# Kernel tuning notes

Measured on AMD Instinct MI355X. Metric: run time of the kernel, lower is better.

## Reference

```python
import jax, jax.numpy as jnp
import numpy as np

EMBED = 512
HEADS = 8
HEAD_DIM = EMBED // HEADS
EPS = 1e-5


def setup_inputs() -> dict:
    key = jax.random.key(0)
    ks = jax.random.split(key, 10)
    s = 1.0 / np.sqrt(EMBED)
    x = jax.random.normal(ks[0], (2, 4096, EMBED), dtype=jnp.float32)
    Wq = jax.random.uniform(ks[1], (EMBED, EMBED), jnp.float32, -s, s)
    bq = jnp.zeros((EMBED,), jnp.float32)
    Wk = jax.random.uniform(ks[2], (EMBED, EMBED), jnp.float32, -s, s)
    bk = jnp.zeros((EMBED,), jnp.float32)
    Wv = jax.random.uniform(ks[3], (EMBED, EMBED), jnp.float32, -s, s)
    bv = jnp.zeros((EMBED,), jnp.float32)
    Wo = jax.random.uniform(ks[4], (EMBED, EMBED), jnp.float32, -s, s)
    bo = jnp.zeros((EMBED,), jnp.float32)
    gamma = jnp.ones((EMBED,), jnp.float32)
    beta = jnp.zeros((EMBED,), jnp.float32)
    return {"x": x, "Wq": Wq, "bq": bq, "Wk": Wk, "bk": bk,
            "Wv": Wv, "bv": bv, "Wo": Wo, "bo": bo,
            "gamma": gamma, "beta": beta}


def reference(x, Wq, bq, Wk, bk, Wv, bv, Wo, bo, gamma, beta):
    b, n, e = x.shape
    def split_heads(t):  # [b,n,e] -> [b,h,n,d]
        return t.reshape(b, n, HEADS, HEAD_DIM).transpose(0, 2, 1, 3)
    q = split_heads(x @ Wq + bq)
    k = split_heads(x @ Wk + bk)
    v = split_heads(x @ Wv + bv)
    energy = jnp.einsum('bhqd,bhkd->bhqk', q, k) * (HEAD_DIM ** -0.5)
    attn = jax.nn.softmax(energy, axis=-1)  # dropout=0.0 (eval)
    out = jnp.einsum('bhqk,bhkd->bhqd', attn, v)
    out = out.transpose(0, 2, 1, 3).reshape(b, n, e)
    out = out @ Wo + bo
    y = x + out
    mu = jnp.mean(y, axis=-1, keepdims=True)
    var = jnp.var(y, axis=-1, keepdims=True)
    return (y - mu) * jax.lax.rsqrt(var + EPS) * gamma + beta
```

## Files before the change

### kernel.cpp

```cpp
#include <hip/hip_runtime.h>
#include <hip/hip_bf16.h>


#define ROWS 8192
#define EMB  512
#define SEQ  4096
#define HEADS 8
#define HD   64
#define QSCALE 0.18033688011112042f

typedef __attribute__((ext_vector_type(8))) short bf16x8;
typedef __attribute__((ext_vector_type(4))) short bf16x4;
typedef __attribute__((ext_vector_type(4))) float f32x4;

__device__ __forceinline__ float bf16_to_f(unsigned short u) {
    union { unsigned int i; float f; } v; v.i = ((unsigned int)u) << 16; return v.f;
}
__device__ __forceinline__ unsigned short f_to_bf16(float f) {
    union { __hip_bfloat16 h; unsigned short u; } v; v.h = __float2bfloat16(f); return v.u;
}
__device__ __forceinline__ unsigned int pack_bf16_trunc(float a, float b) {
    return __builtin_amdgcn_perm(__float_as_uint(b), __float_as_uint(a), 0x07060302u);
}
__device__ __forceinline__ void load_lds16(const void* g, void* l) {
    __builtin_amdgcn_global_load_lds(
        (const __attribute__((address_space(1))) void*)g,
        (__attribute__((address_space(3))) void*)l, 16, 0, 0);
}

__device__ __forceinline__ int detect_fp32(const void* x) {
    const unsigned short* p = (const unsigned short*)x;
    int t = threadIdx.x & 63;
    int cnt = 0;
    #pragma unroll
    for (int i = 0; i < 4; ++i) {
        unsigned short u = p[t * 4 + i];
        int e = (u >> 7) & 0xFF;
        cnt += (e >= 140) ? 1 : 0;
    }
    #pragma unroll
    for (int off = 32; off > 0; off >>= 1) cnt += __shfl_xor(cnt, off, 64);
    return cnt > 16;
}

__global__ __launch_bounds__(256) void prep_kernel(
        const void* __restrict__ x, unsigned short* __restrict__ xb,
        const void* W0, const void* W1, const void* W2, const void* W3,
        unsigned short* __restrict__ Wt,
        const void* b0, const void* b1, const void* b2, const void* b3,
        const void* b4, const void* b5, float* __restrict__ bias_all) {
    int fp32 = detect_fp32(x);
    int bid = blockIdx.x;
    int tid = threadIdx.x;
    if (bid < 4096) {
        if (!fp32) return;
        int i = (bid * 256 + tid) * 4;
        float4 v = *(const float4*)((const float*)x + i);
        ushort4 u = { f_to_bf16(v.x), f_to_bf16(v.y), f_to_bf16(v.z), f_to_bf16(v.w) };
        *(ushort4*)(xb + i) = u;
    } else if (bid < 4352) {
        __shared__ float T[64][65];
        int idx0 = bid - 4096;
        int kt = idx0 & 7, nt = (idx0 >> 3) & 7, mat = idx0 >> 6;
        const void* src = (mat == 0) ? W0 : (mat == 1) ? W1 : (mat == 2) ? W2 : W3;
        for (int ii = 0; ii < 4; ++ii) {
            int idx = tid + ii * 256;
            int i = idx >> 4, j = (idx & 15) * 4;
            size_t g = (size_t)(kt * 64 + i) * 512 + nt * 64 + j;
            if (fp32) {
                float4 v = *(const float4*)((const float*)src + g);
                T[i][j] = v.x; T[i][j+1] = v.y; T[i][j+2] = v.z; T[i][j+3] = v.w;
            } else {
                ushort4 u = *(const ushort4*)((const unsigned short*)src + g);
                T[i][j] = bf16_to_f(u.x); T[i][j+1] = bf16_to_f(u.y);
                T[i][j+2] = bf16_to_f(u.z); T[i][j+3] = bf16_to_f(u.w);
            }
        }
        __syncthreads();
        for (int ii = 0; ii < 2; ++ii) {
            int idx = tid + ii * 256;
            int j = idx >> 3, ch = idx & 7;
            unsigned short pk[8];
            for (int t = 0; t < 8; ++t) pk[t] = f_to_bf16(T[ch * 8 + t][j]);
            *(bf16x8*)&Wt[(size_t)(mat * 512 + nt * 64 + j) * 512 + kt * 64 + ch * 8] = *(bf16x8*)pk;
        }
    } else {
        int idx = (bid - 4352) * 256 + tid;
        int mat = idx >> 9, off = idx & 511;
        const void* src = (mat == 0) ? b0 : (mat == 1) ? b1 : (mat == 2) ? b2 :
                          (mat == 3) ? b3 : (mat == 4) ? b4 : b5;
        float v;
        if (fp32) v = ((const float*)src)[off];
        else      v = bf16_to_f(((const unsigned short*)src)[off]);
        bias_all[idx] = v;
    }
}

template <typename OutT>
__global__ __launch_bounds__(256) void gemm_mfma_kernel(
        const unsigned short* __restrict__ A_conv, const unsigned short* __restrict__ A_raw,
        const unsigned short* __restrict__ Bt,
        const float* __restrict__ bias, OutT* __restrict__ C, int ldc, int scale_cols,
        unsigned short* __restrict__ VtOut) {
    __shared__ __align__(16) unsigned short smemg[2][2][128 * 64];
    const unsigned short* A = detect_fp32(A_raw) ? A_conv : A_raw;
    int tid = threadIdx.x;
    int wave = tid >> 6, lane = tid & 63;
    int l15 = lane & 15, quad = lane >> 4;

    int lin = blockIdx.x + gridDim.x * blockIdx.y;
    int nwg = gridDim.x * gridDim.y;
    int bx, by;
    if (nwg & 7) { bx = blockIdx.x; by = blockIdx.y; }
    else {
        int t = (lin & 7) * (nwg >> 3) + (lin >> 3);
        bx = t % gridDim.x; by = t / gridDim.x;
    }
    int m0 = by * 128, n0 = bx * 128;
    int wm = (wave & 1) * 64, wn = (wave >> 1) * 64;
    bool is_v = (VtOut != nullptr) && (n0 >= 1024);

    int rt = wave * 32 + (lane >> 3);
    int ch = (lane & 7) ^ ((lane >> 3) & 7);
    const unsigned short* ag = A  + (size_t)(m0 + rt) * 512 + ch * 8;
    const unsigned short* bg = Bt + (size_t)(n0 + rt) * 512 + ch * 8;

    f32x4 acc[4][4];
    for (int i = 0; i < 4; ++i) for (int j = 0; j < 4; ++j) acc[i][j] = (f32x4){0.f,0.f,0.f,0.f};

#define GSTAGE(buf, k0) do {                                                      \
        unsigned short* Atb = &smemg[buf][0][0];                                  \
        unsigned short* Bsb = &smemg[buf][1][0];                                  \
        _Pragma("unroll")                                                         \
        for (int j = 0; j < 4; ++j) {                                             \
            load_lds16(ag + (size_t)(j * 8) * 512 + (k0), &Atb[(wave * 32 + j * 8) * 64]); \
            load_lds16(bg + (size_t)(j * 8) * 512 + (k0), &Bsb[(wave * 32 + j * 8) * 64]); \
        }                                                                         \
    } while (0)

    GSTAGE(0, 0);

    for (int s = 0; s < 8; ++s) {
        int cur = s & 1;
        asm volatile("s_waitcnt vmcnt(0)" ::: "memory");
        __builtin_amdgcn_sched_barrier(0);
        asm volatile("s_barrier" ::: "memory");
        __builtin_amdgcn_sched_barrier(0);
        if (s + 1 < 8) GSTAGE(cur ^ 1, (s + 1) * 64);

        const unsigned short* At = &smemg[cur][0][0];
        const unsigned short* Bs = &smemg[cur][1][0];
        #pragma unroll
        for (int ks = 0; ks < 2; ++ks) {
            bf16x8 a[4], b[4];
            #pragma unroll
            for (int f = 0; f < 4; ++f) {
                int pc = ((ks * 4 + quad) ^ (l15 & 7)) * 8;
                a[f] = *(const bf16x8*)&At[(wm + f * 16 + l15) * 64 + pc];
                b[f] = *(const bf16x8*)&Bs[(wn + f * 16 + l15) * 64 + pc];
            }
            if (is_v) {
                #pragma unroll
                for (int fm = 0; fm < 4; ++fm)
                    #pragma unroll
                    for (int fn = 0; fn < 4; ++fn)
                        acc[fm][fn] = __builtin_amdgcn_mfma_f32_16x16x32_bf16(a[fm], b[fn], acc[fm][fn], 0, 0, 0);
            } else {
                #pragma unroll
                for (int fm = 0; fm < 4; ++fm)
                    #pragma unroll
                    for (int fn = 0; fn < 4; ++fn)
                        acc[fm][fn] = __builtin_amdgcn_mfma_f32_16x16x32_bf16(b[fn], a[fm], acc[fm][fn], 0, 0, 0);
            }
        }
        __builtin_amdgcn_sched_barrier(0);
    }
#undef GSTAGE

    __syncthreads();
    unsigned short* LT = &smemg[0][0][0];

    float sc = (n0 < scale_cols) ? QSCALE : 1.f;

    if (is_v) {
        #pragma unroll
        for (int fm = 0; fm < 4; ++fm) {
            #pragma unroll
            for (int fn = 0; fn < 4; ++fn) {
                int dcol = wn + fn * 16 + l15;
                float bia = bias[n0 + dcol];
                int seq0 = wm + fm * 16 + quad * 4;
                ushort4 pk = { f_to_bf16(acc[fm][fn][0] + bia),
                               f_to_bf16(acc[fm][fn][1] + bia),
                               f_to_bf16(acc[fm][fn][2] + bia),
                               f_to_bf16(acc[fm][fn][3] + bia) };
                int c8 = (seq0 >> 2) ^ (dcol & 31);
                *(ushort4*)&LT[dcol * 128 + c8 * 4] = pk;
            }
        }
    } else {
        #pragma unroll
        for (int fm = 0; fm < 4; ++fm) {
            #pragma unroll
            for (int fn = 0; fn < 4; ++fn) {
                int row = wm + fm * 16 + l15;
                int col0 = wn + fn * 16 + quad * 4;
                float4 b4 = *(const float4*)&bias[n0 + col0];
                ushort4 pk = { f_to_bf16((acc[fm][fn][0] + b4.x) * sc),
                               f_to_bf16((acc[fm][fn][1] + b4.y) * sc),
                               f_to_bf16((acc[fm][fn][2] + b4.z) * sc),
                               f_to_bf16((acc[fm][fn][3] + b4.w) * sc) };
                int c8 = (col0 >> 2) ^ (row & 31);
                *(ushort4*)&LT[row * 128 + c8 * 4] = pk;
            }
        }
    }
    __syncthreads();
    #pragma unroll
    for (int i = 0; i < 16; ++i) {
        int row = wave * 32 + i * 2 + (lane >> 5);
        int c8 = lane & 31;
        int phys = c8 ^ (row & 31);
        ushort4 v4 = *(const ushort4*)&LT[row * 128 + phys * 4];
        if (is_v) {
            int hd = n0 - 1024 + row;
            int bh = (m0 >> 12) * 8 + (hd >> 6);
            int d  = hd & 63;
            *(ushort4*)&VtOut[((size_t)(bh * 64 + d)) * SEQ + (m0 & 4095) + c8 * 4] = v4;
        } else {
            *(ushort4*)&C[(size_t)(m0 + row) * ldc + n0 + c8 * 4] = v4;
        }
    }
}

__global__ __launch_bounds__(256, 2) void attn_kernel(
        const unsigned short* __restrict__ QKV, const unsigned short* __restrict__ Vt,
        unsigned short* __restrict__ Ab) {
    __shared__ __align__(16) unsigned char smem[49152];
    float* Ored = (float*)smem;
    float* Lred = (float*)(smem + 16384);

    int tid = threadIdx.x;
    int wave = tid >> 6, lane = tid & 63;
    int l15 = lane & 15, quad = lane >> 4;
    int qh = wave >> 1, kh = wave & 1;
    int lin = blockIdx.x;
    int xcd = lin & 7, slot = lin >> 3;
    int grp = xcd + 8 * (slot >> 5);
    int qt = slot & 31;
    int h = grp & 7, b = grp >> 3;
    int bh = b * HEADS + h;
    size_t qrow0 = (size_t)b * SEQ + qt * 128;

    bf16x8 aq[4][2];
    #pragma unroll
    for (int t = 0; t < 4; ++t) {
        const unsigned short* qp = &QKV[(qrow0 + qh * 64 + t * 16 + l15) * 1536 + h * 64];
        aq[t][0] = *(const bf16x8*)&qp[quad * 8];
        aq[t][1] = *(const bf16x8*)&qp[32 + quad * 8];
    }
    f32x4 o[4][4];
    #pragma unroll
    for (int t = 0; t < 4; ++t)
        #pragma unroll
        for (int db = 0; db < 4; ++db) o[t][db] = (f32x4){0.f, 0.f, 0.f, 0.f};
    f32x4 ol[4];
    #pragma unroll
    for (int t = 0; t < 4; ++t) ol[t] = (f32x4){0.f, 0.f, 0.f, 0.f};
    const bf16x8 ones8 = { (short)0x3F80, (short)0x3F80, (short)0x3F80, (short)0x3F80,
                           (short)0x3F80, (short)0x3F80, (short)0x3F80, (short)0x3F80 };

    int r8 = lane >> 3;
    int kch = (lane & 7) ^ (r8 & 7);
    int r0 = wave * 16 + r8;
    int r1 = wave * 16 + 8 + r8;
    int p0r = (r0 & 32) | (((r0 >> 2) & 3) << 3) | (((r0 >> 4) & 1) << 2) | (r0 & 3);
    int p1r = (r1 & 32) | (((r1 >> 2) & 3) << 3) | (((r1 >> 4) & 1) << 2) | (r1 & 3);
    const unsigned short* kg0 = &QKV[((size_t)b * SEQ + p0r) * 1536 + 512 + h * 64 + kch * 8];
    const unsigned short* kg1 = &QKV[((size_t)b * SEQ + p1r) * 1536 + 512 + h * 64 + kch * 8];
    const unsigned short* vg = &Vt[((size_t)bh * 64 + wave * 16 + r8) * SEQ + kch * 8];

#define STAGE(buf, kt2) do {                                                          \
        unsigned short* Ksb = (unsigned short*)(smem + (buf) * 8192);                 \
        unsigned short* Vsb = (unsigned short*)(smem + 24576 + (buf) * 8192);         \
        load_lds16(kg0 + (size_t)((kt2) * 64) * 1536, &Ksb[(wave * 16) * 64]);        \
        load_lds16(kg1 + (size_t)((kt2) * 64) * 1536, &Ksb[(wave * 16 + 8) * 64]);    \
        load_lds16(vg + (size_t)((kt2) * 64), &Vsb[(wave * 16) * 64]);                \
        load_lds16(vg + (size_t)((kt2) * 64) + (size_t)8 * SEQ,                       \
                   &Vsb[(wave * 16 + 8) * 64]);                                       \
    } while (0)

    STAGE(0, 0);
    STAGE(1, 1);

    int cur = 0;
    for (int kt = 0; kt < SEQ / 64; ++kt) {
        if (kt + 1 < SEQ / 64) {
            asm volatile("s_waitcnt vmcnt(4)" ::: "memory");
        } else {
            asm volatile("s_waitcnt vmcnt(0)" ::: "memory");
        }
        asm volatile("s_barrier" ::: "memory");
        if (kt + 2 < SEQ / 64) {
            int nb2 = cur + 2; if (nb2 >= 3) nb2 -= 3;
            STAGE(nb2, kt + 2);
        }

        const unsigned short* Ksc = (const unsigned short*)(smem + cur * 8192);
        const unsigned short* Vsc = (const unsigned short*)(smem + 24576 + cur * 8192);

        bf16x8 kA[2][2];
        #pragma unroll
        for (int nb = 0; nb < 2; ++nb) {
            int krow = kh * 32 + nb * 16 + l15;
            int key = krow & 7;
            kA[nb][0] = *(const bf16x8*)&Ksc[krow * 64 + (quad ^ key) * 8];
            kA[nb][1] = *(const bf16x8*)&Ksc[krow * 64 + ((4 + quad) ^ key) * 8];
        }
        bf16x8 bv8[4];
        #pragma unroll
        for (int db = 0; db < 4; ++db) {
            int d = db * 16 + l15;
            bv8[db] = *(const bf16x8*)&Vsc[d * 64 + (((kh * 4 + quad) ^ (d & 7))) * 8];
        }
        #pragma unroll
        for (int t = 0; t < 4; ++t) {
            f32x4 sv0 = {0.f, 0.f, 0.f, 0.f};
            f32x4 sv1 = {0.f, 0.f, 0.f, 0.f};
            sv0 = __builtin_amdgcn_mfma_f32_16x16x32_bf16(kA[0][0], aq[t][0], sv0, 0, 0, 0);
            sv0 = __builtin_amdgcn_mfma_f32_16x16x32_bf16(kA[0][1], aq[t][1], sv0, 0, 0, 0);
            sv1 = __builtin_amdgcn_mfma_f32_16x16x32_bf16(kA[1][0], aq[t][0], sv1, 0, 0, 0);
            sv1 = __builtin_amdgcn_mfma_f32_16x16x32_bf16(kA[1][1], aq[t][1], sv1, 0, 0, 0);
            float p0 = __builtin_amdgcn_exp2f(sv0[0]);
            float p1 = __builtin_amdgcn_exp2f(sv0[1]);
            float p2 = __builtin_amdgcn_exp2f(sv0[2]);
            float p3 = __builtin_amdgcn_exp2f(sv0[3]);
            float p4 = __builtin_amdgcn_exp2f(sv1[0]);
            float p5 = __builtin_amdgcn_exp2f(sv1[1]);
            float p6 = __builtin_amdgcn_exp2f(sv1[2]);
            float p7 = __builtin_amdgcn_exp2f(sv1[3]);
            union { unsigned int u[4]; bf16x8 v; } ap;
            ap.u[0] = pack_bf16_trunc(p0, p1);
            ap.u[1] = pack_bf16_trunc(p2, p3);
            ap.u[2] = pack_bf16_trunc(p4, p5);
            ap.u[3] = pack_bf16_trunc(p6, p7);
            #pragma unroll
            for (int db = 0; db < 4; ++db)
                o[t][db] = __builtin_amdgcn_mfma_f32_16x16x32_bf16(ap.v, bv8[db], o[t][db], 0, 0, 0);
            ol[t] = __builtin_amdgcn_mfma_f32_16x16x32_bf16(ap.v, ones8, ol[t], 0, 0, 0);
        }
        cur = (cur == 2) ? 0 : cur + 1;
    }
#undef STAGE

    __syncthreads();
    if (l15 == 0) {
        #pragma unroll
        for (int t = 0; t < 4; ++t)
            #pragma unroll
            for (int r = 0; r < 4; ++r)
                Lred[(wave * 4 + t) * 16 + quad * 4 + r] = ol[t][r];
    }
    __syncthreads();
    float* myO = Ored + wave * (16 * 64);
    #pragma unroll
    for (int t = 0; t < 4; ++t) {
        #pragma unroll
        for (int db = 0; db < 4; ++db)
            #pragma unroll
            for (int r = 0; r < 4; ++r)
                myO[(quad * 4 + r) * 64 + db * 16 + l15] = o[t][db][r];
        __syncthreads();
        {
            int q_l = tid >> 3;
            int dg = tid & 7;
            int qh2 = q_l >> 4, qq = q_l & 15;
            const float* r0p = Ored + (qh2 * 2 + 0) * (16 * 64) + qq * 64 + dg * 8;
            const float* r1p = Ored + (qh2 * 2 + 1) * (16 * 64) + qq * 64 + dg * 8;
            float4 a0 = *(const float4*)&r0p[0];
            float4 a1 = *(const float4*)&r0p[4];
            float4 c0 = *(const float4*)&r1p[0];
            float4 c1 = *(const float4*)&r1p[4];
            float lt = Lred[((qh2 * 2 + 0) * 4 + t) * 16 + qq] +
                       Lred[((qh2 * 2 + 1) * 4 + t) * 16 + qq];
            float inv = 1.f / lt;
            size_t row = qrow0 + qh2 * 64 + t * 16 + qq;
            unsigned short* dst = &Ab[row * EMB + h * 64 + dg * 8];
            ushort4 lo = { f_to_bf16((a0.x + c0.x) * inv), f_to_bf16((a0.y + c0.y) * inv),
                           f_to_bf16((a0.z + c0.z) * inv), f_to_bf16((a0.w + c0.w) * inv) };
            ushort4 hi = { f_to_bf16((a1.x + c1.x) * inv), f_to_bf16((a1.y + c1.y) * inv),
                           f_to_bf16((a1.z + c1.z) * inv), f_to_bf16((a1.w + c1.w) * inv) };
            *(ushort4*)&dst[0] = lo;
            *(ushort4*)&dst[4] = hi;
        }
        __syncthreads();
    }
}

__global__ __launch_bounds__(256) void oproj_ln_kernel(
        const unsigned short* __restrict__ Ab, const unsigned short* __restrict__ Wo,
        const float* __restrict__ bias_all,
        const float* __restrict__ xf, const unsigned short* __restrict__ xraw,
        void* __restrict__ out) {
    __shared__ __align__(16) unsigned short Aslds[32 * 512];
    int fp32 = detect_fp32(xraw);
    int tid = threadIdx.x;
    int wave = tid >> 6, lane = tid & 63;
    int l15 = lane & 15, quad = lane >> 4;
    int m0 = blockIdx.x * 32;

    {
        int c = lane;
        #pragma unroll
        for (int j = 0; j < 8; ++j) {
            int row = j * 4 + wave;
            int csrc = c ^ (row & 7);
            load_lds16(&Ab[(size_t)(m0 + row) * 512 + csrc * 8],
                       &Aslds[row * 512 + c * 8]);
        }
    }
    asm volatile("s_waitcnt vmcnt(0)" ::: "memory");
    __syncthreads();

    f32x4 acc[2][8];
    #pragma unroll
    for (int mf = 0; mf < 2; ++mf)
        #pragma unroll
        for (int nf = 0; nf < 8; ++nf) acc[mf][nf] = (f32x4){0.f, 0.f, 0.f, 0.f};

    const unsigned short* bgl = Wo + (size_t)(wave * 128 + l15) * 512 + quad * 8;

    #pragma unroll
    for (int s = 0; s < 8; ++s) {
        bf16x8 b[2][8];
        #pragma unroll
        for (int ks = 0; ks < 2; ++ks)
            #pragma unroll
            for (int nf = 0; nf < 8; ++nf)
                b[ks][nf] = *(const bf16x8*)&bgl[(size_t)nf * (16 * 512) + s * 64 + ks * 32];
        bf16x8 a[2][2];
        #pragma unroll
        for (int ks = 0; ks < 2; ++ks)
            #pragma unroll
            for (int mf = 0; mf < 2; ++mf) {
                int row = mf * 16 + l15;
                int clog = s * 8 + ks * 4 + quad;
                a[ks][mf] = *(const bf16x8*)&Aslds[row * 512 + (clog ^ (row & 7)) * 8];
            }
        #pragma unroll
        for (int ks = 0; ks < 2; ++ks)
            #pragma unroll
            for (int mf = 0; mf < 2; ++mf)
                #pragma unroll
                for (int nf = 0; nf < 8; ++nf)
                    acc[mf][nf] = __builtin_amdgcn_mfma_f32_16x16x32_bf16(a[ks][mf], b[ks][nf], acc[mf][nf], 0, 0, 0);
    }

    __syncthreads();
    #pragma unroll
    for (int mf = 0; mf < 2; ++mf)
        #pragma unroll
        for (int nf = 0; nf < 8; ++nf) {
            int col = wave * 128 + nf * 16 + l15;
            float bo = bias_all[1536 + col];
            #pragma unroll
            for (int r = 0; r < 4; ++r) {
                int row = mf * 16 + quad * 4 + r;
                Aslds[row * 512 + col] = f_to_bf16(acc[mf][nf][r] + bo);
            }
        }
    __syncthreads();

    const float* gamma = bias_all + 4 * 512;
    const float* beta  = bias_all + 5 * 512;
    float g[8], bt[8];
    #pragma unroll
    for (int i = 0; i < 8; ++i) { g[i] = gamma[lane * 8 + i]; bt[i] = beta[lane * 8 + i]; }

    #pragma unroll
    for (int rr = 0; rr < 8; ++rr) {
        int row = wave * 8 + rr;
        size_t grow = (size_t)(m0 + row);
        const unsigned short* pp = &Aslds[row * 512 + lane * 8];
        ushort4 p0 = *(const ushort4*)&pp[0];
        ushort4 p1 = *(const ushort4*)&pp[4];
        float pv[8] = { bf16_to_f(p0.x), bf16_to_f(p0.y), bf16_to_f(p0.z), bf16_to_f(p0.w),
                        bf16_to_f(p1.x), bf16_to_f(p1.y), bf16_to_f(p1.z), bf16_to_f(p1.w) };
        float v[8];
        if (fp32) {
            const float* xp = &xf[grow * EMB + lane * 8];
            float4 x0 = *(const float4*)&xp[0];
            float4 x1 = *(const float4*)&xp[4];
            v[0] = x0.x + pv[0]; v[1] = x0.y + pv[1]; v[2] = x0.z + pv[2]; v[3] = x0.w + pv[3];
            v[4] = x1.x + pv[4]; v[5] = x1.y + pv[5]; v[6] = x1.z + pv[6]; v[7] = x1.w + pv[7];
        } else {
            const unsigned short* xp = &xraw[grow * EMB + lane * 8];
            ushort4 x0 = *(const ushort4*)&xp[0];
            ushort4 x1 = *(const ushort4*)&xp[4];
            v[0] = bf16_to_f(x0.x) + pv[0]; v[1] = bf16_to_f(x0.y) + pv[1];
            v[2] = bf16_to_f(x0.z) + pv[2]; v[3] = bf16_to_f(x0.w) + pv[3];
            v[4] = bf16_to_f(x1.x) + pv[4]; v[5] = bf16_to_f(x1.y) + pv[5];
            v[6] = bf16_to_f(x1.z) + pv[6]; v[7] = bf16_to_f(x1.w) + pv[7];
        }
        float s = 0.f, ss = 0.f;
        #pragma unroll
        for (int i = 0; i < 8; ++i) { s += v[i]; ss += v[i] * v[i]; }
        #pragma unroll
        for (int off = 32; off > 0; off >>= 1) {
            s  += __shfl_xor(s, off, 64);
            ss += __shfl_xor(ss, off, 64);
        }
        float mu = s * (1.f / 512.f);
        float var = ss * (1.f / 512.f) - mu * mu;
        float rs = rsqrtf(var + 1e-5f);
        if (fp32) {
            float* op = &((float*)out)[grow * EMB + lane * 8];
            float4 o0 = { (v[0] - mu) * rs * g[0] + bt[0], (v[1] - mu) * rs * g[1] + bt[1],
                          (v[2] - mu) * rs * g[2] + bt[2], (v[3] - mu) * rs * g[3] + bt[3] };
            float4 o1 = { (v[4] - mu) * rs * g[4] + bt[4], (v[5] - mu) * rs * g[5] + bt[5],
                          (v[6] - mu) * rs * g[6] + bt[6], (v[7] - mu) * rs * g[7] + bt[7] };
            *(float4*)&op[0] = o0;
            *(float4*)&op[4] = o1;
        } else {
            unsigned short* op = &((unsigned short*)out)[grow * EMB + lane * 8];
            ushort4 o0 = { f_to_bf16((v[0] - mu) * rs * g[0] + bt[0]),
                           f_to_bf16((v[1] - mu) * rs * g[1] + bt[1]),
                           f_to_bf16((v[2] - mu) * rs * g[2] + bt[2]),
                           f_to_bf16((v[3] - mu) * rs * g[3] + bt[3]) };
            ushort4 o1 = { f_to_bf16((v[4] - mu) * rs * g[4] + bt[4]),
                           f_to_bf16((v[5] - mu) * rs * g[5] + bt[5]),
                           f_to_bf16((v[6] - mu) * rs * g[6] + bt[6]),
                           f_to_bf16((v[7] - mu) * rs * g[7] + bt[7]) };
            *(ushort4*)&op[0] = o0;
            *(ushort4*)&op[4] = o1;
        }
    }
}

extern "C" void kernel_launch(void* const* d_in, const int* in_sizes, int n_in,
                              void* d_out, int out_size, void* d_ws, size_t ws_size,
                              hipStream_t stream) {
    char* ws = (char*)d_ws;
    char* p = ws + 256;
    float* bias_all = (float*)p;       p += 6 * 512 * 4;
    unsigned short* Wt   = (unsigned short*)p; p += (size_t)2048 * 512 * 2;
    unsigned short* QKVb = (unsigned short*)p; p += (size_t)ROWS * 1536 * 2;
    unsigned short* Vt   = (unsigned short*)p; p += (size_t)16 * HD * SEQ * 2;
    unsigned short* xb = (unsigned short*)p;
    unsigned short* Ab = (unsigned short*)p;   p += (size_t)ROWS * EMB * 2;

    prep_kernel<<<4364, 256, 0, stream>>>(d_in[0], xb,
        d_in[1], d_in[3], d_in[5], d_in[7], Wt,
        d_in[2], d_in[4], d_in[6], d_in[8], d_in[9], d_in[10], bias_all);

    gemm_mfma_kernel<unsigned short><<<dim3(12, 64), 256, 0, stream>>>(
        xb, (const unsigned short*)d_in[0], Wt, bias_all, QKVb, 1536, 512, Vt);

    attn_kernel<<<dim3(512), 256, 0, stream>>>(QKVb, Vt, Ab);

    oproj_ln_kernel<<<ROWS / 32, 256, 0, stream>>>(
        Ab, Wt + (size_t)1536 * 512, bias_all,
        (const float*)d_in[0], (const unsigned short*)d_in[0], d_out);
}
```

Baseline: 204.7 us.

## Switch attention kernel MFMAs from 16x16x32 to 32x32x16 bf16 tiles

The attention inner loop now uses 32x32x16 MFMA instructions for both the QK^T scores and the PV/row-sum products, replacing 16x16x32 tiles. Q fragments, the K row permutation on load, the LDS read patterns and the epilogue reduction layout are all changed to match the 32-row output layout. Larger MFMA tiles mean fewer instructions and fewer LDS fragment reads per FLOP, at the cost of bigger accumulators (16 floats each), which raises register pressure under the 2-blocks-per-CU launch bound.

```diff
diff --git a/kernel.cpp b/kernel.cpp
--- a/kernel.cpp
+++ b/kernel.cpp
@@ -12,6 +12,9 @@
 typedef __attribute__((ext_vector_type(8))) short bf16x8;
 typedef __attribute__((ext_vector_type(4))) short bf16x4;
 typedef __attribute__((ext_vector_type(4))) float f32x4;
+typedef __attribute__((ext_vector_type(16))) float f32x16;
+
+#define MFMA32(A, B, C) __builtin_amdgcn_mfma_f32_32x32x16_bf16(A, B, C, 0, 0, 0)
 
 __device__ __forceinline__ float bf16_to_f(unsigned short u) {
     union { unsigned int i; float f; } v; v.i = ((unsigned int)u) << 16; return v.f;
@@ -237,47 +240,49 @@
         const unsigned short* __restrict__ QKV, const unsigned short* __restrict__ Vt,
         unsigned short* __restrict__ Ab) {
     __shared__ __align__(16) unsigned char smem[49152];
-    float* Ored = (float*)smem;
-    float* Lred = (float*)(smem + 16384);
 
     int tid = threadIdx.x;
     int wave = tid >> 6, lane = tid & 63;
-    int l15 = lane & 15, quad = lane >> 4;
+    int l31 = lane & 31, lh = lane >> 5;
     int qh = wave >> 1, kh = wave & 1;
     int lin = blockIdx.x;
     int xcd = lin & 7, slot = lin >> 3;
     int grp = xcd + 8 * (slot >> 5);
-    int qt = slot & 31;
+    int qt0 = slot & 31;
     int h = grp & 7, b = grp >> 3;
     int bh = b * HEADS + h;
-    size_t qrow0 = (size_t)b * SEQ + qt * 128;
-
-    bf16x8 aq[4][2];
-    #pragma unroll
-    for (int t = 0; t < 4; ++t) {
-        const unsigned short* qp = &QKV[(qrow0 + qh * 64 + t * 16 + l15) * 1536 + h * 64];
-        aq[t][0] = *(const bf16x8*)&qp[quad * 8];
-        aq[t][1] = *(const bf16x8*)&qp[32 + quad * 8];
-    }
-    f32x4 o[4][4];
-    #pragma unroll
-    for (int t = 0; t < 4; ++t)
-        #pragma unroll
-        for (int db = 0; db < 4; ++db) o[t][db] = (f32x4){0.f, 0.f, 0.f, 0.f};
-    f32x4 ol[4];
-    #pragma unroll
-    for (int t = 0; t < 4; ++t) ol[t] = (f32x4){0.f, 0.f, 0.f, 0.f};
+    size_t qrow0 = (size_t)b * SEQ + qt0 * 128;
+
+    bf16x8 aq[2][4];
+    #pragma unroll
+    for (int qt = 0; qt < 2; ++qt) {
+        const unsigned short* qp = &QKV[(qrow0 + qh * 64 + qt * 32 + l31) * 1536 + h * 64];
+        #pragma unroll
+        for (int ks = 0; ks < 4; ++ks)
+            aq[qt][ks] = *(const bf16x8*)&qp[ks * 16 + lh * 8];
+    }
+    f32x16 o[2][2];
+    f32x16 ol[2];
+    #pragma unroll
+    for (int qt = 0; qt < 2; ++qt) {
+        #pragma unroll
+        for (int dt = 0; dt < 2; ++dt)
+            #pragma unroll
+            for (int i = 0; i < 16; ++i) o[qt][dt][i] = 0.f;
+        #pragma unroll
+        for (int i = 0; i < 16; ++i) ol[qt][i] = 0.f;
+    }
     const bf16x8 ones8 = { (short)0x3F80, (short)0x3F80, (short)0x3F80, (short)0x3F80,
                            (short)0x3F80, (short)0x3F80, (short)0x3F80, (short)0x3F80 };
 
     int r8 = lane >> 3;
     int kch = (lane & 7) ^ (r8 & 7);
-    int r0 = wave * 16 + r8;
-    int r1 = wave * 16 + 8 + r8;
-    int p0r = (r0 & 32) | (((r0 >> 2) & 3) << 3) | (((r0 >> 4) & 1) << 2) | (r0 & 3);
-    int p1r = (r1 & 32) | (((r1 >> 2) & 3) << 3) | (((r1 >> 4) & 1) << 2) | (r1 & 3);
-    const unsigned short* kg0 = &QKV[((size_t)b * SEQ + p0r) * 1536 + 512 + h * 64 + kch * 8];
-    const unsigned short* kg1 = &QKV[((size_t)b * SEQ + p1r) * 1536 + 512 + h * 64 + kch * 8];
+    int p0 = wave * 16 + r8;
+    int p1 = p0 + 8;
+    int s0 = (p0 & ~12) | ((p0 & 4) << 1) | ((p0 & 8) >> 1);
+    int s1 = (p1 & ~12) | ((p1 & 4) << 1) | ((p1 & 8) >> 1);
+    const unsigned short* kg0 = &QKV[((size_t)b * SEQ + s0) * 1536 + 512 + h * 64 + kch * 8];
+    const unsigned short* kg1 = &QKV[((size_t)b * SEQ + s1) * 1536 + 512 + h * 64 + kch * 8];
     const unsigned short* vg = &Vt[((size_t)bh * 64 + wave * 16 + r8) * SEQ + kch * 8];
 
 #define STAGE(buf, kt2) do {                                                          \
@@ -309,89 +314,89 @@
         const unsigned short* Ksc = (const unsigned short*)(smem + cur * 8192);
         const unsigned short* Vsc = (const unsigned short*)(smem + 24576 + cur * 8192);
 
-        bf16x8 kA[2][2];
-        #pragma unroll
-        for (int nb = 0; nb < 2; ++nb) {
-            int krow = kh * 32 + nb * 16 + l15;
-            int key = krow & 7;
-            kA[nb][0] = *(const bf16x8*)&Ksc[krow * 64 + (quad ^ key) * 8];
-            kA[nb][1] = *(const bf16x8*)&Ksc[krow * 64 + ((4 + quad) ^ key) * 8];
-        }
-        bf16x8 bv8[4];
-        #pragma unroll
-        for (int db = 0; db < 4; ++db) {
-            int d = db * 16 + l15;
-            bv8[db] = *(const bf16x8*)&Vsc[d * 64 + (((kh * 4 + quad) ^ (d & 7))) * 8];
-        }
-        #pragma unroll
-        for (int t = 0; t < 4; ++t) {
-            f32x4 sv0 = {0.f, 0.f, 0.f, 0.f};
-            f32x4 sv1 = {0.f, 0.f, 0.f, 0.f};
-            sv0 = __builtin_amdgcn_mfma_f32_16x16x32_bf16(kA[0][0], aq[t][0], sv0, 0, 0, 0);
-            sv0 = __builtin_amdgcn_mfma_f32_16x16x32_bf16(kA[0][1], aq[t][1], sv0, 0, 0, 0);
-            sv1 = __builtin_amdgcn_mfma_f32_16x16x32_bf16(kA[1][0], aq[t][0], sv1, 0, 0, 0);
-            sv1 = __builtin_amdgcn_mfma_f32_16x16x32_bf16(kA[1][1], aq[t][1], sv1, 0, 0, 0);
-            float p0 = __builtin_amdgcn_exp2f(sv0[0]);
-            float p1 = __builtin_amdgcn_exp2f(sv0[1]);
-            float p2 = __builtin_amdgcn_exp2f(sv0[2]);
-            float p3 = __builtin_amdgcn_exp2f(sv0[3]);
-            float p4 = __builtin_amdgcn_exp2f(sv1[0]);
-            float p5 = __builtin_amdgcn_exp2f(sv1[1]);
-            float p6 = __builtin_amdgcn_exp2f(sv1[2]);
-            float p7 = __builtin_amdgcn_exp2f(sv1[3]);
-            union { unsigned int u[4]; bf16x8 v; } ap;
-            ap.u[0] = pack_bf16_trunc(p0, p1);
-            ap.u[1] = pack_bf16_trunc(p2, p3);
-            ap.u[2] = pack_bf16_trunc(p4, p5);
-            ap.u[3] = pack_bf16_trunc(p6, p7);
-            #pragma unroll
-            for (int db = 0; db < 4; ++db)
-                o[t][db] = __builtin_amdgcn_mfma_f32_16x16x32_bf16(ap.v, bv8[db], o[t][db], 0, 0, 0);
-            ol[t] = __builtin_amdgcn_mfma_f32_16x16x32_bf16(ap.v, ones8, ol[t], 0, 0, 0);
-        }
+        bf16x8 kA[4];
+        #pragma unroll
+        for (int ks = 0; ks < 4; ++ks)
+            kA[ks] = *(const bf16x8*)&Ksc[(kh * 32 + l31) * 64 + (((ks * 2 + lh) ^ (lane & 7))) * 8];
+        bf16x8 bv[2][2];
+        #pragma unroll
+        for (int dt = 0; dt < 2; ++dt)
+            #pragma unroll
+            for (int kc = 0; kc < 2; ++kc)
+                bv[dt][kc] = *(const bf16x8*)&Vsc[(dt * 32 + l31) * 64 +
+                                                  (((kh * 4 + kc * 2 + lh) ^ (lane & 7))) * 8];
+
+        bf16x8 ap[2][2];
+        #pragma unroll
+        for (int qt = 0; qt < 2; ++qt) {
+            f32x16 sv;
+            #pragma unroll
+            for (int i = 0; i < 16; ++i) sv[i] = 0.f;
+            #pragma unroll
+            for (int ks = 0; ks < 4; ++ks)
+                sv = MFMA32(kA[ks], aq[qt][ks], sv);
+            float p[16];
+            #pragma unroll
+            for (int i = 0; i < 16; ++i) p[i] = __builtin_amdgcn_exp2f(sv[i]);
+            union { unsigned int u[4]; bf16x8 v; } a0, a1;
+            #pragma unroll
+            for (int j = 0; j < 4; ++j) {
+                a0.u[j] = pack_bf16_trunc(p[2 * j], p[2 * j + 1]);
+                a1.u[j] = pack_bf16_trunc(p[8 + 2 * j], p[8 + 2 * j + 1]);
+            }
+            ap[qt][0] = a0.v;
+            ap[qt][1] = a1.v;
+            ol[qt] = MFMA32(ap[qt][0], ones8, ol[qt]);
+            ol[qt] = MFMA32(ap[qt][1], ones8, ol[qt]);
+        }
+        #pragma unroll
+        for (int qt = 0; qt < 2; ++qt)
+            #pragma unroll
+            for (int dt = 0; dt < 2; ++dt) {
+                o[qt][dt] = MFMA32(ap[qt][0], bv[dt][0], o[qt][dt]);
+                o[qt][dt] = MFMA32(ap[qt][1], bv[dt][1], o[qt][dt]);
+            }
         cur = (cur == 2) ? 0 : cur + 1;
     }
 #undef STAGE
 
     __syncthreads();
-    if (l15 == 0) {
-        #pragma unroll
-        for (int t = 0; t < 4; ++t)
-            #pragma unroll
-            for (int r = 0; r < 4; ++r)
-                Lred[(wave * 4 + t) * 16 + quad * 4 + r] = ol[t][r];
-    }
-    __syncthreads();
-    float* myO = Ored + wave * (16 * 64);
-    #pragma unroll
-    for (int t = 0; t < 4; ++t) {
-        #pragma unroll
-        for (int db = 0; db < 4; ++db)
-            #pragma unroll
-            for (int r = 0; r < 4; ++r)
-                myO[(quad * 4 + r) * 64 + db * 16 + l15] = o[t][db][r];
+    float* Ored = (float*)smem;
+    float* Lred = (float*)(smem + 32768);
+    if (l31 == 0) {
+        #pragma unroll
+        for (int qt = 0; qt < 2; ++qt)
+            #pragma unroll
+            for (int r = 0; r < 16; ++r)
+                Lred[(wave * 2 + qt) * 32 + (r & 3) + 8 * (r >> 2) + 4 * lh] = ol[qt][r];
+    }
+    #pragma unroll
+    for (int qt = 0; qt < 2; ++qt) {
+        #pragma unroll
+        for (int dt = 0; dt < 2; ++dt)
+            #pragma unroll
+            for (int r = 0; r < 16; ++r)
+                Ored[wave * 2048 + ((r & 3) + 8 * (r >> 2) + 4 * lh) * 64 + dt * 32 + l31]
+                    = o[qt][dt][r];
         __syncthreads();
         {
-            int q_l = tid >> 3;
-            int dg = tid & 7;
-            int qh2 = q_l >> 4, qq = q_l & 15;
-            const float* r0p = Ored + (qh2 * 2 + 0) * (16 * 64) + qq * 64 + dg * 8;
-            const float* r1p = Ored + (qh2 * 2 + 1) * (16 * 64) + qq * 64 + dg * 8;
-            float4 a0 = *(const float4*)&r0p[0];
-            float4 a1 = *(const float4*)&r0p[4];
-            float4 c0 = *(const float4*)&r1p[0];
-            float4 c1 = *(const float4*)&r1p[4];
-            float lt = Lred[((qh2 * 2 + 0) * 4 + t) * 16 + qq] +
-                       Lred[((qh2 * 2 + 1) * 4 + t) * 16 + qq];
+            int row6 = tid >> 2, dq = tid & 3;
+            int qh2 = row6 >> 5, qq = row6 & 31;
+            const float* r0p = Ored + (qh2 * 2 + 0) * 2048 + qq * 64 + dq * 16;
+            const float* r1p = Ored + (qh2 * 2 + 1) * 2048 + qq * 64 + dq * 16;
+            float lt = Lred[((qh2 * 2 + 0) * 2 + qt) * 32 + qq] +
+                       Lred[((qh2 * 2 + 1) * 2 + qt) * 32 + qq];
             float inv = 1.f / lt;
-            size_t row = qrow0 + qh2 * 64 + t * 16 + qq;
-            unsigned short* dst = &Ab[row * EMB + h * 64 + dg * 8];
-            ushort4 lo = { f_to_bf16((a0.x + c0.x) * inv), f_to_bf16((a0.y + c0.y) * inv),
-                           f_to_bf16((a0.z + c0.z) * inv), f_to_bf16((a0.w + c0.w) * inv) };
-            ushort4 hi = { f_to_bf16((a1.x + c1.x) * inv), f_to_bf16((a1.y + c1.y) * inv),
-                           f_to_bf16((a1.z + c1.z) * inv), f_to_bf16((a1.w + c1.w) * inv) };
-            *(ushort4*)&dst[0] = lo;
-            *(ushort4*)&dst[4] = hi;
+            size_t row = qrow0 + qh2 * 64 + qt * 32 + qq;
+            unsigned short* dst = &Ab[row * EMB + h * 64 + dq * 16];
+            #pragma unroll
+            for (int i = 0; i < 4; ++i) {
+                float4 a = *(const float4*)&r0p[i * 4];
+                float4 c = *(const float4*)&r1p[i * 4];
+                ushort4 pk = { f_to_bf16((a.x + c.x) * inv), f_to_bf16((a.y + c.y) * inv),
+                               f_to_bf16((a.z + c.z) * inv), f_to_bf16((a.w + c.w) * inv) };
+                *(ushort4*)&dst[i * 4] = pk;
+            }
         }
         __syncthreads();
     }
```

After: 214.8 us. +4.9%, slower.
